# Kernel tuning notes

Measured on AMD Instinct MI355X. Metric: run time of the kernel, lower is better.

Reference implementation:

```python
import jax, jax.numpy as jnp
import numpy as np

NEG_SLOPE = 0.2
EPS_SOFTMAX = 1e-16
EPS_NORM = 1e-12
H = 4


def gat_conv(x, src, dst, edge_attr, W, att_src, att_dst, W_edge, att_edge, bias, concat):
    """PyG GATConv with edge_dim, add_self_loops=False.
    x: [N, F_in]; src,dst: [E]; edge_attr: [E, edge_dim]
    W: [F_in, H*C]; att_src/att_dst/att_edge: [H, C]; W_edge: [edge_dim, H*C]
    """
    N = x.shape[0]
    C = att_src.shape[1]
    xs = (x @ W).reshape(N, H, C)                      # [N,H,C]
    a_s = jnp.einsum('nhc,hc->nh', xs, att_src)        # [N,H]
    a_d = jnp.einsum('nhc,hc->nh', xs, att_dst)        # [N,H]
    e = (edge_attr @ W_edge).reshape(-1, H, C)         # [E,H,C]
    a_e = jnp.einsum('ehc,hc->eh', e, att_edge)        # [E,H]
    alpha = a_s[src] + a_d[dst] + a_e                  # [E,H]
    alpha = jax.nn.leaky_relu(alpha, NEG_SLOPE)
    # segment softmax over edges grouped by destination node
    m = jax.ops.segment_max(alpha, dst, num_segments=N)        # [N,H]
    ex = jnp.exp(alpha - m[dst])
    denom = jax.ops.segment_sum(ex, dst, num_segments=N)       # [N,H]
    alpha = ex / (denom[dst] + EPS_SOFTMAX)
    # message = attention-weighted source features, scatter-add to dst
    out = jax.ops.segment_sum(xs[src] * alpha[..., None], dst, num_segments=N)  # [N,H,C]
    out = out.reshape(N, H * C) if concat else out.mean(axis=1)
    return out + bias


def l2_normalize(x):
    n = jnp.linalg.norm(x, axis=-1, keepdims=True)
    return x / jnp.maximum(n, EPS_NORM)


def setup_inputs() -> dict:
    key = jax.random.key(0)
    ks = jax.random.split(key, 16)
    N, E, F_in, C1, C2 = 50000, 800000, 128, 64, 64
    glorot = lambda k, shape: jax.random.uniform(
        k, shape, jnp.float32, -1.0, 1.0) * np.sqrt(6.0 / (shape[0] + shape[-1]))
    return {
        'x': jax.random.normal(ks[0], (N, F_in), jnp.float32),
        'edge_index': jax.random.randint(ks[1], (2, E), 0, N, jnp.int32),
        'edge_weight': jax.random.uniform(ks[2], (E, 1), jnp.float32),
        # layer 1: in=128 -> H*C1=256, concat=True
        'W1': glorot(ks[3], (F_in, H * C1)),
        'att_src1': glorot(ks[4], (H, C1)),
        'att_dst1': glorot(ks[5], (H, C1)),
        'We1': glorot(ks[6], (1, H * C1)),
        'att_e1': glorot(ks[7], (H, C1)),
        'b1': jnp.zeros((H * C1,), jnp.float32),
        # layer 2: in=256 -> H*C2, concat=False (mean over heads)
        'W2': glorot(ks[8], (H * C1, H * C2)),
        'att_src2': glorot(ks[9], (H, C2)),
        'att_dst2': glorot(ks[10], (H, C2)),
        'We2': glorot(ks[11], (1, H * C2)),
        'att_e2': glorot(ks[12], (H, C2)),
        'b2': jnp.zeros((C2,), jnp.float32),
    }


def reference(x, edge_index, edge_weight, W1, att_src1, att_dst1, We1, att_e1, b1,
              W2, att_src2, att_dst2, We2, att_e2, b2):
    src, dst = edge_index[0], edge_index[1]
    h = gat_conv(x, src, dst, edge_weight, W1, att_src1, att_dst1, We1, att_e1, b1, concat=True)
    h = jax.nn.relu(l2_normalize(h))
    out = gat_conv(h, src, dst, edge_weight, W2, att_src2, att_dst2, We2, att_e2, b2, concat=False)
    return out
```

## Files before the change

kernel.cpp:

```cpp
#include <hip/hip_runtime.h>
#include <hip/hip_bf16.h>

typedef unsigned short u16;
typedef unsigned long long u64;
using bf16x8 = __attribute__((ext_vector_type(8))) short;
using f32x4v = __attribute__((ext_vector_type(4))) float;
typedef float v2f __attribute__((ext_vector_type(2)));

#define HC 256
#define CDIM 64

__device__ __forceinline__ float b2f(u16 u){
  union { unsigned int i; float f; } c; c.i = ((unsigned)u) << 16; return c.f;
}
__device__ __forceinline__ u16 f2b(float f){
  union { float f; unsigned int i; } c; c.f = f;
  unsigned int x = c.i;
  return (u16)((x + 0x7FFFu + ((x >> 16) & 1u)) >> 16);
}
__device__ __forceinline__ float ldf(const void* p, size_t i, int isbf){
  return isbf ? b2f(((const u16*)p)[i]) : ((const float*)p)[i];
}
__device__ __forceinline__ float sel4(float4 v, int h){ return h==0?v.x:(h==1?v.y:(h==2?v.z:v.w)); }
__device__ __forceinline__ float lrelu(float v){ return v>0.f ? v : 0.2f*v; }

__device__ __forceinline__ void glds16(const void* g, void* l){
  __builtin_amdgcn_global_load_lds(
      (const __attribute__((address_space(1))) unsigned int*)g,
      (__attribute__((address_space(3))) unsigned int*)l, 16, 0, 0);
}

__device__ __forceinline__ float4 wave_max4(float4 m){
  #pragma unroll
  for(int o=32;o>0;o>>=1){
    m.x=fmaxf(m.x,__shfl_xor(m.x,o));
    m.y=fmaxf(m.y,__shfl_xor(m.y,o));
    m.z=fmaxf(m.z,__shfl_xor(m.z,o));
    m.w=fmaxf(m.w,__shfl_xor(m.w,o));
  }
  return m;
}
__device__ __forceinline__ float4 wave_sum4(float4 m){
  #pragma unroll
  for(int o=32;o>0;o>>=1){
    m.x+=__shfl_xor(m.x,o);
    m.y+=__shfl_xor(m.y,o);
    m.z+=__shfl_xor(m.z,o);
    m.w+=__shfl_xor(m.w,o);
  }
  return m;
}

__global__ __launch_bounds__(256) void k_hist_prep(
    const int* __restrict__ dst, int E, int N, int* __restrict__ deg,
    int* __restrict__ rank,
    const u16* __restrict__ x, int nelem, int* __restrict__ flag,
    const void* __restrict__ W1, const void* __restrict__ W2,
    const void* __restrict__ We1, const void* __restrict__ ae1,
    const void* __restrict__ We2, const void* __restrict__ ae2,
    u16* __restrict__ Bt1, u16* __restrict__ Bt2, float* __restrict__ ce){
  int eb = (E + 255) >> 8;
  int t = threadIdx.x;
  if ((int)blockIdx.x < eb){
    int e = blockIdx.x*256 + t;
    if (e < E){
      int d = dst[e];
      if ((unsigned)d < (unsigned)N) rank[e] = atomicAdd(&deg[d], 1);
    }
    if (blockIdx.x == 0){
      __shared__ int bad0;
      if (t==0) bad0 = 0;
      __syncthreads();
      int n = nelem < 8192 ? nelem : 8192;
      int lb = 0;
      for (int i=t; i<n; i+=256){
        int ex = (x[i] >> 7) & 0xFF;
        if (ex >= 140) lb++;
      }
      if (lb) atomicAdd(&bad0, 1);
      __syncthreads();
      if (t==0) *flag = (bad0==0) ? 1 : 0;
    }
    return;
  }
  __shared__ int bad;
  if (t==0) bad = 0;
  __syncthreads();
  {
    int n = nelem < 8192 ? nelem : 8192;
    int lb = 0;
    for (int i=t; i<n; i+=256){
      int ex = (x[i] >> 7) & 0xFF;
      if (ex >= 140) lb++;
    }
    if (lb) atomicAdd(&bad, 1);
  }
  __syncthreads();
  int bf = (bad==0) ? 1 : 0;
  int b = blockIdx.x - eb;
  if (b < 128){
    Bt1[(size_t)t*128 + b] = f2b(ldf(W1, (size_t)b*HC + t, bf));
  } else if (b < 384){
    int k = b - 128;
    Bt2[(size_t)t*256 + k] = f2b(ldf(W2, (size_t)k*HC + t, bf));
  } else {
    float p1 = ldf(We1, t, bf)*ldf(ae1, t, bf);
    float p2 = ldf(We2, t, bf)*ldf(ae2, t, bf);
    #pragma unroll
    for(int o=32;o>0;o>>=1){ p1+=__shfl_xor(p1,o); p2+=__shfl_xor(p2,o); }
    if((t&63)==0){ ce[t>>6]=p1; ce[4+(t>>6)]=p2; }
  }
}

__global__ void k_scan1(const int* __restrict__ in, int* __restrict__ out, int* __restrict__ bsums, int n){
  __shared__ int s[256];
  int t = threadIdx.x;
  int i = blockIdx.x*256 + t;
  int v = (i<n)? in[i] : 0;
  s[t]=v; __syncthreads();
  for(int off=1; off<256; off<<=1){
    int tv = (t>=off)? s[t-off] : 0;
    __syncthreads();
    s[t]+=tv; __syncthreads();
  }
  if (i<n) out[i] = s[t]-v;
  if (t==255) bsums[blockIdx.x] = s[255];
}

__global__ void k_scan2(int* __restrict__ bsums, int nb){
  __shared__ int s[256];
  int t=threadIdx.x;
  int v=(t<nb)? bsums[t]:0;
  s[t]=v; __syncthreads();
  for(int off=1; off<256; off<<=1){
    int tv=(t>=off)? s[t-off]:0;
    __syncthreads();
    s[t]+=tv; __syncthreads();
  }
  if (t<nb) bsums[t]=s[t]-v;
}

__device__ __forceinline__ void scatter_body(int sb, const int* __restrict__ srcv,
    const int* __restrict__ dst, const void* __restrict__ ew, int E, int N,
    const int* __restrict__ rowptr, const int* __restrict__ bsums, const int* __restrict__ rank,
    u64* __restrict__ epk, int bf){
  int e = sb*256 + threadIdx.x;
  if (e>=E) return;
  int d = dst[e];
  if ((unsigned)d >= (unsigned)N) return;
  int p = rowptr[d] + bsums[d>>8] + rank[e];
  int s = srcv[e];
  if ((unsigned)s >= (unsigned)N) s = 0;
  u64 v = ((u64)__float_as_uint(ldf(ew, e, bf)) << 32) | (unsigned)s;
  __builtin_nontemporal_store(v, &epk[p]);
}

__device__ __forceinline__ void gemm_body(int bidx,
    const void* __restrict__ A, int a_ext, const u16* __restrict__ Bt,
    u16* __restrict__ C, const void* __restrict__ att_s, const void* __restrict__ att_d,
    float* __restrict__ a_s, float* __restrict__ a_d,
    int M, int K, int bf)
{
  __shared__ u16 sh[64*264];
  __shared__ float att_sh[512];
  u16* As = sh;
  u16* Bs = sh + 2048;
  int a_bf = a_ext ? bf : 1;
  int tid = threadIdx.x;
  int lane = tid & 63, w = tid >> 6;
  int quad = lane >> 4, ln = lane & 15;
  int m0 = bidx * 64;
  bool adma = (!a_ext) || (a_bf && (m0 + 64 <= M));

  att_sh[tid]       = ldf(att_s, tid, bf);
  att_sh[256 + tid] = ldf(att_d, tid, bf);

  f32x4v acc[4][4] = {};
  for (int k0 = 0; k0 < K; k0 += 32){
    if (adma){
      const u16* gA = (const u16*)A + (size_t)(m0 + (tid>>2))*K + k0 + (size_t)(tid&3)*8;
      glds16(gA, (char*)As + (size_t)w*1024);
    } else {
      int m = tid >> 2, g = tid & 3;
      int r = m0 + m;
      uint4 pack;
      if (r < M){
        size_t base = (size_t)r*K + k0 + g*8;
        if (a_bf){
          pack = *(const uint4*)((const u16*)A + base);
        } else {
          const float* Af = (const float*)A + base;
          float4 f0 = *(const float4*)Af;
          float4 f1 = *(const float4*)(Af+4);
          unsigned a0 = (unsigned)f2b(f0.x) | ((unsigned)f2b(f0.y)<<16);
          unsigned a1 = (unsigned)f2b(f0.z) | ((unsigned)f2b(f0.w)<<16);
          unsigned a2 = (unsigned)f2b(f1.x) | ((unsigned)f2b(f1.y)<<16);
          unsigned a3 = (unsigned)f2b(f1.z) | ((unsigned)f2b(f1.w)<<16);
          pack = make_uint4(a0,a1,a2,a3);
        }
      } else pack = make_uint4(0,0,0,0);
      ((uint4*)As)[tid] = pack;
    }
    #pragma unroll
    for (int i=0;i<4;i++){
      const u16* gB = Bt + (size_t)(i*64 + (tid>>2))*K + k0 + (size_t)(tid&3)*8;
      glds16(gB, (char*)Bs + (size_t)i*4096 + (size_t)w*1024);
    }
    __syncthreads();
    bf16x8 af[4], bfr[4];
    #pragma unroll
    for (int mi=0;mi<4;mi++) af[mi] = *(const bf16x8*)&As[(mi*16+ln)*32 + quad*8];
    #pragma unroll
    for (int nj=0;nj<4;nj++) bfr[nj] = *(const bf16x8*)&Bs[((size_t)w*64+nj*16+ln)*32 + quad*8];
    #pragma unroll
    for (int mi=0;mi<4;mi++)
      #pragma unroll
      for (int nj=0;nj<4;nj++)
        acc[mi][nj] = __builtin_amdgcn_mfma_f32_16x16x32_bf16(af[mi], bfr[nj], acc[mi][nj], 0,0,0);
    __syncthreads();
  }
  #pragma unroll
  for (int mi=0;mi<4;mi++)
    #pragma unroll
    for (int nj=0;nj<4;nj++){
      union { __hip_bfloat162 h2; u16 u[2]; } cv0, cv1;
      cv0.h2 = __float22bfloat162_rn(make_float2(acc[mi][nj][0], acc[mi][nj][1]));
      cv1.h2 = __float22bfloat162_rn(make_float2(acc[mi][nj][2], acc[mi][nj][3]));
      int col = w*64 + nj*16 + ln;
      int rbase = mi*16 + quad*4;
      sh[(rbase+0)*264 + col] = cv0.u[0];
      sh[(rbase+1)*264 + col] = cv0.u[1];
      sh[(rbase+2)*264 + col] = cv1.u[0];
      sh[(rbase+3)*264 + col] = cv1.u[1];
    }
  __syncthreads();
  #pragma unroll
  for (int j=0;j<8;j++){
    int idx = j*256 + tid;
    int r = idx >> 5, gq = idx & 31;
    if (m0 + r < M)
      *(uint4*)(C + (size_t)(m0+r)*HC + gq*8) = *(const uint4*)&sh[r*264 + gq*8];
  }
  {
    int r  = w*16 + ln;
    int hh = quad;
    const u16* crow = &sh[r*264 + hh*64];
    const float* asv = &att_sh[hh*64];
    const float* adv = &att_sh[256 + hh*64];
    float ps = 0.f, pd = 0.f;
    #pragma unroll
    for (int cb=0; cb<64; cb+=8){
      ushort4 ua = *(const ushort4*)&crow[cb];
      ushort4 ub = *(const ushort4*)&crow[cb+4];
      float4 sa = *(const float4*)&asv[cb];
      float4 sb = *(const float4*)&asv[cb+4];
      float4 da = *(const float4*)&adv[cb];
      float4 db = *(const float4*)&adv[cb+4];
      float c0=b2f(ua.x), c1=b2f(ua.y), c2=b2f(ua.z), c3=b2f(ua.w);
      float c4=b2f(ub.x), c5=b2f(ub.y), c6=b2f(ub.z), c7=b2f(ub.w);
      ps += c0*sa.x + c1*sa.y + c2*sa.z + c3*sa.w + c4*sb.x + c5*sb.y + c6*sb.z + c7*sb.w;
      pd += c0*da.x + c1*da.y + c2*da.z + c3*da.w + c4*db.x + c5*db.y + c6*db.z + c7*db.w;
    }
    if (m0 + r < M){
      a_s[(size_t)(m0+r)*4 + hh] = ps;
      a_d[(size_t)(m0+r)*4 + hh] = pd;
    }
  }
}

__global__ __launch_bounds__(256) void k_gemm_mfma(
    const void* __restrict__ A, int a_ext, const u16* __restrict__ Bt,
    u16* __restrict__ C, const void* __restrict__ att_s, const void* __restrict__ att_d,
    float* __restrict__ a_s, float* __restrict__ a_d,
    int M, int K, const int* __restrict__ flagp){
  gemm_body(blockIdx.x, A, a_ext, Bt, C, att_s, att_d, a_s, a_d, M, K, *flagp);
}

__global__ __launch_bounds__(256) void k_gemm_scatter(
    const void* __restrict__ A, const u16* __restrict__ Bt,
    u16* __restrict__ C, const void* __restrict__ att_s, const void* __restrict__ att_d,
    float* __restrict__ a_s, float* __restrict__ a_d,
    int M, int K, const int* __restrict__ flagp, int gemmBlocks,
    const int* __restrict__ srcv, const int* __restrict__ dst, const void* __restrict__ ew,
    int E, const int* __restrict__ rowptr, const int* __restrict__ bsums,
    const int* __restrict__ rank, u64* __restrict__ epk){
  int bf = *flagp;
  if ((int)blockIdx.x < gemmBlocks){
    gemm_body(blockIdx.x, A, 1, Bt, C, att_s, att_d, a_s, a_d, M, K, bf);
  } else {
    scatter_body(blockIdx.x - gemmBlocks, srcv, dst, ew, E, M, rowptr, bsums, rank, epk, bf);
  }
}

#define GRP4(E0, TWJ) { \
  int s0_=__builtin_amdgcn_readlane(s_reg,(E0)+0); \
  int s1_=__builtin_amdgcn_readlane(s_reg,(E0)+1); \
  int s2_=__builtin_amdgcn_readlane(s_reg,(E0)+2); \
  int s3_=__builtin_amdgcn_readlane(s_reg,(E0)+3); \
  uint2 x0_=*(const uint2*)&xs[(size_t)s0_*HC + (lane<<2)]; \
  uint2 x1_=*(const uint2*)&xs[(size_t)s1_*HC + (lane<<2)]; \
  uint2 x2_=*(const uint2*)&xs[(size_t)s2_*HC + (lane<<2)]; \
  uint2 x3_=*(const uint2*)&xs[(size_t)s3_*HC + (lane<<2)]; \
  float w0_=__shfl((TWJ), ibase+(((E0)+0)&15)); \
  float w1_=__shfl((TWJ), ibase+(((E0)+1)&15)); \
  float w2_=__shfl((TWJ), ibase+(((E0)+2)&15)); \
  float w3_=__shfl((TWJ), ibase+(((E0)+3)&15)); \
  v2f f_; \
  f_=(v2f){__uint_as_float(x0_.x<<16),__uint_as_float(x0_.x&0xFFFF0000u)}; a01+=f_*w0_; \
  f_=(v2f){__uint_as_float(x0_.y<<16),__uint_as_float(x0_.y&0xFFFF0000u)}; a23+=f_*w0_; \
  f_=(v2f){__uint_as_float(x1_.x<<16),__uint_as_float(x1_.x&0xFFFF0000u)}; a01+=f_*w1_; \
  f_=(v2f){__uint_as_float(x1_.y<<16),__uint_as_float(x1_.y&0xFFFF0000u)}; a23+=f_*w1_; \
  f_=(v2f){__uint_as_float(x2_.x<<16),__uint_as_float(x2_.x&0xFFFF0000u)}; a01+=f_*w2_; \
  f_=(v2f){__uint_as_float(x2_.y<<16),__uint_as_float(x2_.y&0xFFFF0000u)}; a23+=f_*w2_; \
  f_=(v2f){__uint_as_float(x3_.x<<16),__uint_as_float(x3_.x&0xFFFF0000u)}; a01+=f_*w3_; \
  f_=(v2f){__uint_as_float(x3_.y<<16),__uint_as_float(x3_.y&0xFFFF0000u)}; a23+=f_*w3_; \
}

__global__ __launch_bounds__(256) void k_soft_agg(
    const u16* __restrict__ xs, const int* __restrict__ rowptr, const int* __restrict__ bsums,
    const int* __restrict__ deg, const u64* __restrict__ epk,
    const float* __restrict__ a_s, const float* __restrict__ a_d, const float* __restrict__ ce4,
    const void* __restrict__ bias, void* __restrict__ outp, int N, int layer,
    const int* __restrict__ flagp){
  int bf = *flagp;
  int lane = threadIdx.x & 63;
  int w = threadIdx.x >> 6;
  int n = (blockIdx.x<<2) + w;
  if (n >= N) return;
  int row = rowptr[n] + bsums[n>>8];
  int dg = deg[n];
  float4 ad = *(const float4*)&a_d[(size_t)n*4];
  float4 ce = *(const float4*)ce4;
  int h = lane >> 4;
  float4 acc = make_float4(0.f,0.f,0.f,0.f);
  if (dg > 0){
    if (dg <= 64){
      u64 pk = 0;
      if (lane < dg) pk = epk[row + lane];
      int s = (int)(unsigned)(pk & 0xFFFFFFFFull);
      if ((unsigned)s >= (unsigned)N) s = 0;
      int s_reg = s;
      float wv = __uint_as_float((unsigned)(pk >> 32));
      float4 as4 = *(const float4*)&a_s[(size_t)s*4];
      uint2 xpf[16];
      #pragma unroll
      for (int k=0;k<16;k++){
        int sk = __builtin_amdgcn_readlane(s_reg, k);
        xpf[k] = *(const uint2*)&xs[(size_t)sk*HC + (lane<<2)];
      }
      bool vlane = lane < dg;
      float4 ex;
      ex.x = vlane ? __expf(lrelu(as4.x+ad.x+wv*ce.x)) : 0.f;
      ex.y = vlane ? __expf(lrelu(as4.y+ad.y+wv*ce.y)) : 0.f;
      ex.z = vlane ? __expf(lrelu(as4.z+ad.z+wv*ce.z)) : 0.f;
      ex.w = vlane ? __expf(lrelu(as4.w+ad.w+wv*ce.w)) : 0.f;
      float4 ss = ex;
      if (dg > 32){
        ss.x+=__shfl_xor(ss.x,32); ss.y+=__shfl_xor(ss.y,32);
        ss.z+=__shfl_xor(ss.z,32); ss.w+=__shfl_xor(ss.w,32);
      }
      if (dg > 16){
        ss.x+=__shfl_xor(ss.x,16); ss.y+=__shfl_xor(ss.y,16);
        ss.z+=__shfl_xor(ss.z,16); ss.w+=__shfl_xor(ss.w,16);
      }
      #pragma unroll
      for(int o=8;o>0;o>>=1){
        ss.x+=__shfl_xor(ss.x,o); ss.y+=__shfl_xor(ss.y,o);
        ss.z+=__shfl_xor(ss.z,o); ss.w+=__shfl_xor(ss.w,o);
      }
      float4 wgt;
      wgt.x = ex.x/(ss.x+1e-16f); wgt.y = ex.y/(ss.y+1e-16f);
      wgt.z = ex.z/(ss.z+1e-16f); wgt.w = ex.w/(ss.w+1e-16f);
      int ibase = lane & 48;
      float tw0, tw1, tw2, tw3;
      {
        int srcl = lane & 15;
        float c0=__shfl(wgt.x,srcl), c1=__shfl(wgt.y,srcl);
        float c2=__shfl(wgt.z,srcl), c3=__shfl(wgt.w,srcl);
        tw0 = (h==0)?c0:((h==1)?c1:((h==2)?c2:c3));
      }
      if (dg > 16){
        int srcl = 16 + (lane & 15);
        float c0=__shfl(wgt.x,srcl), c1=__shfl(wgt.y,srcl);
        float c2=__shfl(wgt.z,srcl), c3=__shfl(wgt.w,srcl);
        tw1 = (h==0)?c0:((h==1)?c1:((h==2)?c2:c3));
      } else tw1 = 0.f;
      if (dg > 32){
        int srcl = 32 + (lane & 15);
        float c0=__shfl(wgt.x,srcl), c1=__shfl(wgt.y,srcl);
        float c2=__shfl(wgt.z,srcl), c3=__shfl(wgt.w,srcl);
        tw2 = (h==0)?c0:((h==1)?c1:((h==2)?c2:c3));
      } else tw2 = 0.f;
      if (dg > 48){
        int srcl = 48 + (lane & 15);
        float c0=__shfl(wgt.x,srcl), c1=__shfl(wgt.y,srcl);
        float c2=__shfl(wgt.z,srcl), c3=__shfl(wgt.w,srcl);
        tw3 = (h==0)?c0:((h==1)?c1:((h==2)?c2:c3));
      } else tw3 = 0.f;
      v2f a01 = {0.f,0.f}, a23 = {0.f,0.f};
      #pragma unroll
      for (int k=0;k<16;k++){
        float wk = __shfl(tw0, ibase+k);
        uint2 xv = xpf[k];
        v2f f;
        f = (v2f){__uint_as_float(xv.x<<16), __uint_as_float(xv.x&0xFFFF0000u)}; a01 += f*wk;
        f = (v2f){__uint_as_float(xv.y<<16), __uint_as_float(xv.y&0xFFFF0000u)}; a23 += f*wk;
      }
      if (dg > 16){
        GRP4(16, tw1);
        if (dg > 20) GRP4(20, tw1);
        if (dg > 24) GRP4(24, tw1);
        if (dg > 28) GRP4(28, tw1);
        if (dg > 32){
          GRP4(32, tw2);
          if (dg > 36) GRP4(36, tw2);
          if (dg > 40) GRP4(40, tw2);
          if (dg > 44) GRP4(44, tw2);
          if (dg > 48){
            GRP4(48, tw3);
            if (dg > 52) GRP4(52, tw3);
            if (dg > 56) GRP4(56, tw3);
            if (dg > 60) GRP4(60, tw3);
          }
        }
      }
      acc.x = a01.x; acc.y = a01.y; acc.z = a23.x; acc.w = a23.y;
    } else {
      float4 m = make_float4(-1e30f,-1e30f,-1e30f,-1e30f);
      for (int p=lane;p<dg;p+=64){
        u64 pk = epk[row+p];
        int s = (int)(unsigned)(pk & 0xFFFFFFFFull);
        if ((unsigned)s >= (unsigned)N) s = 0;
        float wv = __uint_as_float((unsigned)(pk >> 32));
        float4 as = *(const float4*)&a_s[(size_t)s*4];
        m.x=fmaxf(m.x, lrelu(as.x+ad.x+wv*ce.x));
        m.y=fmaxf(m.y, lrelu(as.y+ad.y+wv*ce.y));
        m.z=fmaxf(m.z, lrelu(as.z+ad.z+wv*ce.z));
        m.w=fmaxf(m.w, lrelu(as.w+ad.w+wv*ce.w));
      }
      m = wave_max4(m);
      float4 ss = make_float4(0.f,0.f,0.f,0.f);
      for (int p=lane;p<dg;p+=64){
        u64 pk = epk[row+p];
        int s = (int)(unsigned)(pk & 0xFFFFFFFFull);
        if ((unsigned)s >= (unsigned)N) s = 0;
        float wv = __uint_as_float((unsigned)(pk >> 32));
        float4 as = *(const float4*)&a_s[(size_t)s*4];
        ss.x+=__expf(lrelu(as.x+ad.x+wv*ce.x)-m.x);
        ss.y+=__expf(lrelu(as.y+ad.y+wv*ce.y)-m.y);
        ss.z+=__expf(lrelu(as.z+ad.z+wv*ce.z)-m.z);
        ss.w+=__expf(lrelu(as.w+ad.w+wv*ce.w)-m.w);
      }
      ss = wave_sum4(ss);
      float rsel=1.f/(sel4(ss,h)+1e-16f), mh=sel4(m,h), adh=sel4(ad,h), ceh=sel4(ce,h);
      for (int e=0;e<dg;e++){
        u64 pk = epk[row+e];
        int s = (int)(unsigned)(pk & 0xFFFFFFFFull);
        if ((unsigned)s >= (unsigned)N) s = 0;
        float wv = __uint_as_float((unsigned)(pk >> 32));
        float arv = lrelu(a_s[(size_t)s*4+h]+adh+wv*ceh);
        float wgt = __expf(arv-mh)*rsel;
        ushort4 xv4 = *(const ushort4*)&xs[(size_t)s*HC + lane*4];
        acc.x+=wgt*b2f(xv4.x); acc.y+=wgt*b2f(xv4.y);
        acc.z+=wgt*b2f(xv4.z); acc.w+=wgt*b2f(xv4.w);
      }
    }
  }
  if (layer==1){
    float4 v;
    v.x = acc.x + ldf(bias, lane*4+0, bf);
    v.y = acc.y + ldf(bias, lane*4+1, bf);
    v.z = acc.z + ldf(bias, lane*4+2, bf);
    v.w = acc.w + ldf(bias, lane*4+3, bf);
    float ss = v.x*v.x+v.y*v.y+v.z*v.z+v.w*v.w;
    #pragma unroll
    for(int o=32;o>0;o>>=1) ss += __shfl_xor(ss,o);
    float inv = 1.f/fmaxf(sqrtf(ss), 1e-12f);
    ushort4 o4;
    o4.x = f2b(fmaxf(v.x*inv,0.f)); o4.y = f2b(fmaxf(v.y*inv,0.f));
    o4.z = f2b(fmaxf(v.z*inv,0.f)); o4.w = f2b(fmaxf(v.w*inv,0.f));
    *(ushort4*)((u16*)outp + (size_t)n*HC + lane*4) = o4;
  } else {
    float4 s = acc;
    #pragma unroll
    for (int o=16;o<=32;o<<=1){
      s.x+=__shfl_xor(s.x,o); s.y+=__shfl_xor(s.y,o);
      s.z+=__shfl_xor(s.z,o); s.w+=__shfl_xor(s.w,o);
    }
    if (lane < 16){
      float4 v;
      v.x = 0.25f*s.x + ldf(bias, lane*4+0, bf);
      v.y = 0.25f*s.y + ldf(bias, lane*4+1, bf);
      v.z = 0.25f*s.z + ldf(bias, lane*4+2, bf);
      v.w = 0.25f*s.w + ldf(bias, lane*4+3, bf);
      if (bf){
        ushort4 o4; o4.x=f2b(v.x); o4.y=f2b(v.y); o4.z=f2b(v.z); o4.w=f2b(v.w);
        *(ushort4*)((u16*)outp + (size_t)n*CDIM + lane*4) = o4;
      } else {
        *(float4*)((float*)outp + (size_t)n*CDIM + lane*4) = v;
      }
    }
  }
}

extern "C" void kernel_launch(void* const* d_in, const int* in_sizes, int n_in,
                              void* d_out, int out_size, void* d_ws, size_t ws_size,
                              hipStream_t stream){
  const void* x_in = d_in[0];
  const int* eidx  = (const int*)d_in[1];
  const void* ew   = d_in[2];
  const void* W1   = d_in[3];
  const void* as1  = d_in[4];
  const void* ad1  = d_in[5];
  const void* We1  = d_in[6];
  const void* ae1  = d_in[7];
  const void* b1   = d_in[8];
  const void* W2   = d_in[9];
  const void* as2  = d_in[10];
  const void* ad2  = d_in[11];
  const void* We2  = d_in[12];
  const void* ae2  = d_in[13];
  const void* b2   = d_in[14];

  int N = in_sizes[0]/128;
  int E = in_sizes[2];
  const int* srcp = eidx;
  const int* dstp = eidx + E;

  char* w = (char*)d_ws;
  auto alloc = [&](size_t bytes)->char*{ char* p=w; w += (bytes+255)/256*256; return p; };
  int*   flag  = (int*)alloc(256);
  u16*   xs    = (u16*)alloc((size_t)N*HC*2);
  u16*   hbuf  = (u16*)alloc((size_t)N*HC*2);
  float* a_s   = (float*)alloc((size_t)N*4*4);
  float* a_d   = (float*)alloc((size_t)N*4*4);
  int*   deg   = (int*)alloc((size_t)N*4);
  int*   rowptr= (int*)alloc((size_t)N*4);
  int*   bsums = (int*)alloc(256*4);
  int*   rank  = (int*)alloc((size_t)E*4);
  u64*   epk   = (u64*)alloc((size_t)E*8);
  float* ce    = (float*)alloc(256);
  u16*   Bt1   = (u16*)alloc((size_t)HC*128*2);
  u16*   Bt2   = (u16*)alloc((size_t)HC*HC*2);

  (void)hipMemsetAsync(deg, 0, (size_t)N*4, stream);

  int eb = (E+255)/256;
  int nb = (N+255)/256;
  int nelem = in_sizes[0];
  k_hist_prep<<<eb+385,256,0,stream>>>(dstp, E, N, deg, rank, (const u16*)x_in, nelem, flag,
                                       W1, W2, We1, ae1, We2, ae2, Bt1, Bt2, ce);
  k_scan1<<<nb,256,0,stream>>>(deg, rowptr, bsums, N);
  k_scan2<<<1,256,0,stream>>>(bsums, nb);

  int gemmBlocks = (N+63)/64;
  int nwb = (N+3)/4;

  k_gemm_scatter<<<gemmBlocks+eb,256,0,stream>>>(x_in, Bt1, xs, as1, ad1, a_s, a_d, N, 128, flag,
                                                 gemmBlocks, srcp, dstp, ew, E, rowptr, bsums, rank, epk);
  k_soft_agg<<<nwb,256,0,stream>>>(xs, rowptr, bsums, deg, epk, a_s, a_d, ce, b1, hbuf, N, 1, flag);

  k_gemm_mfma<<<gemmBlocks,256,0,stream>>>(hbuf, 0, Bt2, xs, as2, ad2, a_s, a_d, N, 256, flag);
  k_soft_agg<<<nwb,256,0,stream>>>(xs, rowptr, bsums, deg, epk, a_s, a_d, ce+4, b2, d_out, N, 2, flag);
}
```

Before: 316.0 us.

## Fuse two-pass scan into single kernel and remap GEMM LDS tile layout

The two-kernel prefix scan is replaced by one kernel in which each block recomputes its global offset by summing all preceding degrees. This removes a launch and the bsums indirection in the scatter and aggregation kernels. The GEMM tile load mapping and LDS read addressing are also changed so each wave stages 16 full rows, giving contiguous 8-element fragment reads and fewer bank conflicts. The cost is that later scan blocks redundantly read up to N degree values, which is quadratic-ish total work (~196 blocks × up to 50k reads).

After: 345.6 us. +9.4%, slower.

```diff
diff --git a/kernel.cpp b/kernel.cpp
--- a/kernel.cpp
+++ b/kernel.cpp
@@ -112,43 +112,39 @@
   }
 }
 
-__global__ void k_scan1(const int* __restrict__ in, int* __restrict__ out, int* __restrict__ bsums, int n){
+__global__ __launch_bounds__(256) void k_scan(const int* __restrict__ deg,
+                                              int* __restrict__ rowptr, int N){
   __shared__ int s[256];
-  int t = threadIdx.x;
-  int i = blockIdx.x*256 + t;
-  int v = (i<n)? in[i] : 0;
+  __shared__ int wred[4];
+  int t = threadIdx.x, c = blockIdx.x;
+  int base = c << 8;
+  int part = 0;
+  for (int i = t; i < base; i += 256) part += deg[i];
+  #pragma unroll
+  for (int o=32;o>0;o>>=1) part += __shfl_xor(part,o);
+  if ((t&63)==0) wred[t>>6] = part;
+  __syncthreads();
+  int offset = wred[0]+wred[1]+wred[2]+wred[3];
+  int i = base + t;
+  int v = (i<N)? deg[i] : 0;
   s[t]=v; __syncthreads();
   for(int off=1; off<256; off<<=1){
     int tv = (t>=off)? s[t-off] : 0;
     __syncthreads();
     s[t]+=tv; __syncthreads();
   }
-  if (i<n) out[i] = s[t]-v;
-  if (t==255) bsums[blockIdx.x] = s[255];
-}
-
-__global__ void k_scan2(int* __restrict__ bsums, int nb){
-  __shared__ int s[256];
-  int t=threadIdx.x;
-  int v=(t<nb)? bsums[t]:0;
-  s[t]=v; __syncthreads();
-  for(int off=1; off<256; off<<=1){
-    int tv=(t>=off)? s[t-off]:0;
-    __syncthreads();
-    s[t]+=tv; __syncthreads();
-  }
-  if (t<nb) bsums[t]=s[t]-v;
+  if (i<N) rowptr[i] = s[t]-v + offset;
 }
 
 __device__ __forceinline__ void scatter_body(int sb, const int* __restrict__ srcv,
     const int* __restrict__ dst, const void* __restrict__ ew, int E, int N,
-    const int* __restrict__ rowptr, const int* __restrict__ bsums, const int* __restrict__ rank,
+    const int* __restrict__ rowptr, const int* __restrict__ rank,
     u64* __restrict__ epk, int bf){
   int e = sb*256 + threadIdx.x;
   if (e>=E) return;
   int d = dst[e];
   if ((unsigned)d >= (unsigned)N) return;
-  int p = rowptr[d] + bsums[d>>8] + rank[e];
+  int p = rowptr[d] + rank[e];
   int s = srcv[e];
   if ((unsigned)s >= (unsigned)N) s = 0;
   u64 v = ((u64)__float_as_uint(ldf(ew, e, bf)) << 32) | (unsigned)s;
@@ -171,6 +167,8 @@
   int quad = lane >> 4, ln = lane & 15;
   int m0 = bidx * 64;
   bool adma = (!a_ext) || (a_bf && (m0 + 64 <= M));
+  int srow = lane & 15;
+  int sg   = lane >> 4;
 
   att_sh[tid]       = ldf(att_s, tid, bf);
   att_sh[256 + tid] = ldf(att_d, tid, bf);
@@ -178,14 +176,13 @@
   f32x4v acc[4][4] = {};
   for (int k0 = 0; k0 < K; k0 += 32){
     if (adma){
-      const u16* gA = (const u16*)A + (size_t)(m0 + (tid>>2))*K + k0 + (size_t)(tid&3)*8;
+      const u16* gA = (const u16*)A + (size_t)(m0 + w*16 + srow)*K + k0 + (size_t)sg*8;
       glds16(gA, (char*)As + (size_t)w*1024);
     } else {
-      int m = tid >> 2, g = tid & 3;
-      int r = m0 + m;
+      int r = m0 + w*16 + srow;
       uint4 pack;
       if (r < M){
-        size_t base = (size_t)r*K + k0 + g*8;
+        size_t base = (size_t)r*K + k0 + sg*8;
         if (a_bf){
           pack = *(const uint4*)((const u16*)A + base);
         } else {
@@ -203,15 +200,15 @@
     }
     #pragma unroll
     for (int i=0;i<4;i++){
-      const u16* gB = Bt + (size_t)(i*64 + (tid>>2))*K + k0 + (size_t)(tid&3)*8;
+      const u16* gB = Bt + (size_t)(i*64 + w*16 + srow)*K + k0 + (size_t)sg*8;
       glds16(gB, (char*)Bs + (size_t)i*4096 + (size_t)w*1024);
     }
     __syncthreads();
     bf16x8 af[4], bfr[4];
     #pragma unroll
-    for (int mi=0;mi<4;mi++) af[mi] = *(const bf16x8*)&As[(mi*16+ln)*32 + quad*8];
-    #pragma unroll
-    for (int nj=0;nj<4;nj++) bfr[nj] = *(const bf16x8*)&Bs[((size_t)w*64+nj*16+ln)*32 + quad*8];
+    for (int mi=0;mi<4;mi++) af[mi] = *(const bf16x8*)&As[mi*512 + quad*128 + ln*8];
+    #pragma unroll
+    for (int nj=0;nj<4;nj++) bfr[nj] = *(const bf16x8*)&Bs[((size_t)(w*4+nj))*512 + quad*128 + ln*8];
     #pragma unroll
     for (int mi=0;mi<4;mi++)
       #pragma unroll
@@ -282,13 +279,12 @@
     float* __restrict__ a_s, float* __restrict__ a_d,
     int M, int K, const int* __restrict__ flagp, int gemmBlocks,
     const int* __restrict__ srcv, const int* __restrict__ dst, const void* __restrict__ ew,
-    int E, const int* __restrict__ rowptr, const int* __restrict__ bsums,
-    const int* __restrict__ rank, u64* __restrict__ epk){
+    int E, const int* __restrict__ rowptr, const int* __restrict__ rank, u64* __restrict__ epk){
   int bf = *flagp;
   if ((int)blockIdx.x < gemmBlocks){
     gemm_body(blockIdx.x, A, 1, Bt, C, att_s, att_d, a_s, a_d, M, K, bf);
   } else {
-    scatter_body(blockIdx.x - gemmBlocks, srcv, dst, ew, E, M, rowptr, bsums, rank, epk, bf);
+    scatter_body(blockIdx.x - gemmBlocks, srcv, dst, ew, E, M, rowptr, rank, epk, bf);
   }
 }
 
@@ -317,7 +313,7 @@
 }
 
 __global__ __launch_bounds__(256) void k_soft_agg(
-    const u16* __restrict__ xs, const int* __restrict__ rowptr, const int* __restrict__ bsums,
+    const u16* __restrict__ xs, const int* __restrict__ rowptr,
     const int* __restrict__ deg, const u64* __restrict__ epk,
     const float* __restrict__ a_s, const float* __restrict__ a_d, const float* __restrict__ ce4,
     const void* __restrict__ bias, void* __restrict__ outp, int N, int layer,
@@ -327,7 +323,7 @@
   int w = threadIdx.x >> 6;
   int n = (blockIdx.x<<2) + w;
   if (n >= N) return;
-  int row = rowptr[n] + bsums[n>>8];
+  int row = rowptr[n];
   int dg = deg[n];
   float4 ad = *(const float4*)&a_d[(size_t)n*4];
   float4 ce = *(const float4*)ce4;
@@ -536,7 +532,6 @@
   float* a_d   = (float*)alloc((size_t)N*4*4);
   int*   deg   = (int*)alloc((size_t)N*4);
   int*   rowptr= (int*)alloc((size_t)N*4);
-  int*   bsums = (int*)alloc(256*4);
   int*   rank  = (int*)alloc((size_t)E*4);
   u64*   epk   = (u64*)alloc((size_t)E*8);
   float* ce    = (float*)alloc(256);
@@ -550,16 +545,15 @@
   int nelem = in_sizes[0];
   k_hist_prep<<<eb+385,256,0,stream>>>(dstp, E, N, deg, rank, (const u16*)x_in, nelem, flag,
                                        W1, W2, We1, ae1, We2, ae2, Bt1, Bt2, ce);
-  k_scan1<<<nb,256,0,stream>>>(deg, rowptr, bsums, N);
-  k_scan2<<<1,256,0,stream>>>(bsums, nb);
+  k_scan<<<nb,256,0,stream>>>(deg, rowptr, N);
 
   int gemmBlocks = (N+63)/64;
   int nwb = (N+3)/4;
 
   k_gemm_scatter<<<gemmBlocks+eb,256,0,stream>>>(x_in, Bt1, xs, as1, ad1, a_s, a_d, N, 128, flag,
-                                                 gemmBlocks, srcp, dstp, ew, E, rowptr, bsums, rank, epk);
-  k_soft_agg<<<nwb,256,0,stream>>>(xs, rowptr, bsums, deg, epk, a_s, a_d, ce, b1, hbuf, N, 1, flag);
+                                                 gemmBlocks, srcp, dstp, ew, E, rowptr, rank, epk);
+  k_soft_agg<<<nwb,256,0,stream>>>(xs, rowptr, deg, epk, a_s, a_d, ce, b1, hbuf, N, 1, flag);
 
   k_gemm_mfma<<<gemmBlocks,256,0,stream>>>(hbuf, 0, Bt2, xs, as2, ad2, a_s, a_d, N, 256, flag);
-  k_soft_agg<<<nwb,256,0,stream>>>(xs, rowptr, bsums, deg, epk, a_s, a_d, ce+4, b2, d_out, N, 2, flag);
-}
+  k_soft_agg<<<nwb,256,0,stream>>>(xs, rowptr, deg, epk, a_s, a_d, ce+4, b2, d_out, N, 2, flag);
+}
```
